# Performance work log

Hardware: AMD Instinct MI355X
Metric: run time of the kernel (lower is better)

The kernel has to match this reference:

```python
import jax, jax.numpy as jnp
import numpy as np

D = 128
N = 300000
M = 262144
LN_EPS = 1e-5


def setup_inputs() -> dict:
    key = jax.random.key(0)
    ks = jax.random.split(key, 20)
    inp = {
        'h_p': jax.random.normal(ks[0], (N, D), jnp.float32),
        'h_k': jax.random.normal(ks[1], (N, D), jnp.float32),
        'h_o': jax.random.normal(ks[2], (M, D), jnp.float32),
        'weight_o': jax.random.normal(ks[3], (D, D // 2), jnp.float32) * 0.15,
        'weight_p': jax.random.normal(ks[4], (D, D // 2), jnp.float32) * 0.15,
        'lin_W': jax.random.normal(ks[5], (D, D), jnp.float32) * 0.08,
        'lin_b': jax.random.normal(ks[6], (D,), jnp.float32) * 0.05,
        'bias': jax.random.normal(ks[7], (D,), jnp.float32) * 0.05,
        'Wq': jax.random.normal(ks[8], (D, D), jnp.float32) * 0.08,
        'bq': jax.random.normal(ks[9], (D,), jnp.float32) * 0.05,
        'Wk': jax.random.normal(ks[10], (D, D), jnp.float32) * 0.08,
        'bk': jax.random.normal(ks[11], (D,), jnp.float32) * 0.05,
        'Wv': jax.random.normal(ks[12], (D, D), jnp.float32) * 0.08,
        'bv': jax.random.normal(ks[13], (D,), jnp.float32) * 0.05,
        'W1': jax.random.normal(ks[14], (D, D), jnp.float32) * 0.08,
        'b1': jax.random.normal(ks[15], (D,), jnp.float32) * 0.05,
        'ln_g': jnp.ones((D,), jnp.float32),
        'ln_b': jnp.zeros((D,), jnp.float32),
        'mutual_index_p': jax.random.randint(ks[16], (M,), 0, N, jnp.int32),
        'mutual_index_k': jax.random.randint(ks[17], (M,), 0, N, jnp.int32),
        'propagation_node_num': N,
        'knowledge_node_num': N,
    }
    return inp


def reference(h_p, h_k, h_o, weight_o, weight_p, lin_W, lin_b, bias,
              Wq, bq, Wk, bk, Wv, bv, W1, b1, ln_g, ln_b,
              mutual_index_p, mutual_index_k,
              propagation_node_num, knowledge_node_num):
    # gather: Q from h_o rows, K from paired h_p/h_k rows (seq len 2)
    ho_sel = h_o[mutual_index_p]                       # [M, D]
    q = ho_sel[:, None, :]                             # [M, 1, D]
    k_in = jnp.stack([h_p[mutual_index_p], h_k[mutual_index_k]], axis=1)  # [M, 2, D]

    Q = q @ Wq.T + bq                                  # [M, 1, D]
    K = k_in @ Wk.T + bk                               # [M, 2, D]
    V = k_in @ Wv.T + bv                               # [M, 2, D]

    scale = jnp.float32(D) ** -0.5
    attn = jax.nn.softmax(jnp.einsum('mqd,mkd->mqk', Q, K) * scale, axis=-1)  # [M,1,2]
    ctx = jnp.einsum('mqk,mkd->mqd', attn, V)          # [M, 1, D]

    fusion = ctx @ W1.T + b1                           # dropout is identity in eval
    mu = jnp.mean(fusion, axis=-1, keepdims=True)
    var = jnp.var(fusion, axis=-1, keepdims=True)
    fusion = (fusion - mu) * jax.lax.rsqrt(var + LN_EPS) * ln_g + ln_b
    fusion = fusion[:, 0, :]                           # [M, D]

    trans_ho = ho_sel @ weight_o                       # [M, D/2]
    trans_pk = fusion @ weight_p                       # [M, D/2]
    out = jnp.tanh(jnp.concatenate([trans_ho, trans_pk], axis=1))
    out = jax.nn.leaky_relu(out @ lin_W.T + lin_b, negative_slope=0.01)
    out = out + bias                                   # [M, D]

    h_p = h_p.at[mutual_index_p].set(out)
    h_k = h_k.at[mutual_index_k].set(out)
    return (h_p, h_k)
```

## Files before the change

### kernel.cpp

```cpp
#include <hip/hip_runtime.h>
#include <stdint.h>

#define D 128
#define NROWS 300000
#define MIDX 262144
#define SBH 132
#define WAVE_BUF (16 * SBH)

typedef __attribute__((ext_vector_type(8))) short short8_t;
typedef __attribute__((ext_vector_type(4))) short short4_t;
typedef __attribute__((ext_vector_type(4))) float float4v;

__device__ __forceinline__ short f2bf(float x) {
  uint32_t u = __float_as_uint(x);
  u = (u + 0x7FFFu + ((u >> 16) & 1u)) >> 16;
  return (short)u;
}

__global__ void winners_kernel(const int* __restrict__ idx_p,
                               const int* __restrict__ idx_k,
                               int* __restrict__ wp, int* __restrict__ wk) {
  int m = blockIdx.x * 256 + threadIdx.x;
  if (m < MIDX) {
    atomicMax(&wp[idx_p[m]], m);
    atomicMax(&wk[idx_k[m]], m);
  }
}

__global__ __launch_bounds__(256)
void copyrest_kernel(const float* __restrict__ h_p, const float* __restrict__ h_k,
                     const int* __restrict__ wp, const int* __restrict__ wk,
                     float* __restrict__ out_p, float* __restrict__ out_k) {
  int g = blockIdx.x * 256 + threadIdx.x;
  int row = g >> 5;
  if (row >= NROWS) return;
  int c = (g & 31) << 2;
  size_t off = (size_t)row * D + c;
  if (wp[row] < 0) *(float4v*)(out_p + off) = *(const float4v*)(h_p + off);
  if (wk[row] < 0) *(float4v*)(out_k + off) = *(const float4v*)(h_k + off);
}

__global__ void pack_kernel(const float* __restrict__ Wq, const float* __restrict__ Wk,
                            const float* __restrict__ Wv, const float* __restrict__ W1,
                            const float* __restrict__ Wl, const float* __restrict__ Wo,
                            const float* __restrict__ Wp, short* __restrict__ dst) {
  int slot = blockIdx.x;
  int lane = threadIdx.x;
  const float* W; int base; int trans; int rel;
  if      (slot < 32)  { W = Wq; base = 0;     trans = 1; rel = slot; }
  else if (slot < 64)  { W = Wk; base = 16384; trans = 1; rel = slot - 32; }
  else if (slot < 96)  { W = Wv; base = 32768; trans = 1; rel = slot - 64; }
  else if (slot < 128) { W = W1; base = 49152; trans = 1; rel = slot - 96; }
  else if (slot < 160) { W = Wl; base = 65536; trans = 1; rel = slot - 128; }
  else if (slot < 176) { W = Wo; base = 81920; trans = 0; rel = slot - 160; }
  else                 { W = Wp; base = 90112; trans = 0; rel = slot - 176; }
  int t = rel >> 2, s = rel & 3;
  int n = 16 * t + (lane & 15);
  int kb = 32 * s + 8 * (lane >> 4);
  short* o = dst + base + (size_t)(rel * 64 + lane) * 8;
  #pragma unroll
  for (int j = 0; j < 8; j++) {
    float v = trans ? W[n * 128 + kb + j] : W[(kb + j) * 64 + n];
    o[j] = f2bf(v);
  }
}

__device__ __forceinline__ float4v gemm_tile(const short8_t a[4], const short* __restrict__ B,
                                             int t, int lane) {
  float4v acc = {0.f, 0.f, 0.f, 0.f};
  #pragma unroll
  for (int s = 0; s < 4; s++) {
    short8_t b = *(const short8_t*)(B + (size_t)((t * 4 + s) * 64 + lane) * 8);
    acc = __builtin_amdgcn_mfma_f32_16x16x32_bf16(a[s], b, acc, 0, 0, 0);
  }
  return acc;
}

__device__ __forceinline__ void load_row_frags(const float* __restrict__ row, int q, short8_t out[4]) {
  #pragma unroll
  for (int s = 0; s < 4; s++) {
    float4v v0 = *(const float4v*)(row + 32 * s + 8 * q);
    float4v v1 = *(const float4v*)(row + 32 * s + 8 * q + 4);
    short8_t r;
    r[0] = f2bf(v0[0]); r[1] = f2bf(v0[1]); r[2] = f2bf(v0[2]); r[3] = f2bf(v0[3]);
    r[4] = f2bf(v1[0]); r[5] = f2bf(v1[1]); r[6] = f2bf(v1[2]); r[7] = f2bf(v1[3]);
    out[s] = r;
  }
}

__device__ __forceinline__ void read_a_frags(const short* __restrict__ sb, int l15, int q, short8_t out[4]) {
  #pragma unroll
  for (int s = 0; s < 4; s++) {
    const short* p = sb + l15 * SBH + 32 * s + 8 * q;
    short4_t lo = *(const short4_t*)p;
    short4_t hi = *(const short4_t*)(p + 4);
    short8_t v;
    v[0] = lo[0]; v[1] = lo[1]; v[2] = lo[2]; v[3] = lo[3];
    v[4] = hi[0]; v[5] = hi[1]; v[6] = hi[2]; v[7] = hi[3];
    out[s] = v;
  }
}

__device__ __forceinline__ float red16(float v) {
  v += __shfl_xor(v, 1);
  v += __shfl_xor(v, 2);
  v += __shfl_xor(v, 4);
  v += __shfl_xor(v, 8);
  return v;
}

__global__ __launch_bounds__(256, 2)
void fused_kernel(const float* __restrict__ h_p, const float* __restrict__ h_k,
                  const float* __restrict__ h_o, int ho_rows,
                  const int* __restrict__ idx_p, const int* __restrict__ idx_k,
                  const short* __restrict__ wbuf,
                  const float* __restrict__ bq, const float* __restrict__ bk,
                  const float* __restrict__ bv, const float* __restrict__ b1,
                  const float* __restrict__ linb, const float* __restrict__ bias,
                  const float* __restrict__ lng, const float* __restrict__ lnb,
                  const int* __restrict__ wp, const int* __restrict__ wk,
                  float* __restrict__ out_p, float* __restrict__ out_k)
{
  const short* Bq_ = wbuf;
  const short* Bk_ = wbuf + 16384;
  const short* Bv_ = wbuf + 32768;
  const short* B1_ = wbuf + 49152;
  const short* Bl_ = wbuf + 65536;
  const short* Bo_ = wbuf + 81920;
  const short* Bp_ = wbuf + 90112;

  __shared__ float smem[4 * WAVE_BUF];
  const int tid  = threadIdx.x;
  const int wave = tid >> 6;
  const int lane = tid & 63;
  const int l15  = lane & 15;
  const int q    = lane >> 4;

  float* fbuf = smem + wave * WAVE_BUF;
  short* sbuf = (short*)fbuf;

  const int m0   = blockIdx.x * 64 + wave * 16;
  const int mrow = m0 + l15;
  const int ip = idx_p[mrow];
  const int ik = idx_k[mrow];
  const int ipo = (ip < ho_rows) ? ip : (ho_rows - 1);

  short8_t aho[4], ahp[4], ahk[4];
  load_row_frags(h_o + (size_t)ipo * D, q, aho);
  load_row_frags(h_p + (size_t)ip * D, q, ahp);
  load_row_frags(h_k + (size_t)ik * D, q, ahk);

  float4v Q[8];
  #pragma unroll
  for (int t = 0; t < 8; t++) {
    Q[t] = gemm_tile(aho, Bq_, t, lane) + bq[16 * t + l15];
  }

  float4v p0 = {0,0,0,0}, p1 = {0,0,0,0};
  #pragma unroll
  for (int t = 0; t < 8; t++) {
    float bkv = bk[16 * t + l15];
    float4v k0 = gemm_tile(ahp, Bk_, t, lane) + bkv;
    float4v k1 = gemm_tile(ahk, Bk_, t, lane) + bkv;
    p0 += Q[t] * k0;
    p1 += Q[t] * k1;
  }
  float a0[4], a1[4];
  #pragma unroll
  for (int r = 0; r < 4; r++) {
    float s0 = red16(p0[r]) * 0.08838834764831845f;
    float s1 = red16(p1[r]) * 0.08838834764831845f;
    float mx = fmaxf(s0, s1);
    float e0 = __expf(s0 - mx), e1 = __expf(s1 - mx);
    float inv = 1.0f / (e0 + e1);
    a0[r] = e0 * inv;
    a1[r] = e1 * inv;
  }

  float4v ctx[8];
  #pragma unroll
  for (int t = 0; t < 8; t++) {
    float bvv = bv[16 * t + l15];
    float4v v0 = gemm_tile(ahp, Bv_, t, lane) + bvv;
    float4v v1 = gemm_tile(ahk, Bv_, t, lane) + bvv;
    float4v c;
    #pragma unroll
    for (int r = 0; r < 4; r++) c[r] = a0[r] * v0[r] + a1[r] * v1[r];
    ctx[t] = c;
  }

  #pragma unroll
  for (int t = 0; t < 8; t++)
    #pragma unroll
    for (int r = 0; r < 4; r++)
      sbuf[(4 * q + r) * SBH + 16 * t + l15] = f2bf(ctx[t][r]);
  short8_t afu[4];
  read_a_frags(sbuf, l15, q, afu);

  float4v F[8];
  float4v sum = {0,0,0,0}, ssq = {0,0,0,0};
  #pragma unroll
  for (int t = 0; t < 8; t++) {
    float4v f = gemm_tile(afu, B1_, t, lane) + b1[16 * t + l15];
    F[t] = f;
    sum += f;
    ssq += f * f;
  }
  #pragma unroll
  for (int r = 0; r < 4; r++) {
    float s  = red16(sum[r]);
    float s2 = red16(ssq[r]);
    float mu  = s * (1.0f / 128.0f);
    float var = s2 * (1.0f / 128.0f) - mu * mu;
    float rs  = rsqrtf(var + 1e-5f);
    #pragma unroll
    for (int t = 0; t < 8; t++) F[t][r] = (F[t][r] - mu) * rs;
  }
  #pragma unroll
  for (int t = 0; t < 8; t++) {
    int col = 16 * t + l15;
    float g = lng[col], b = lnb[col];
    #pragma unroll
    for (int r = 0; r < 4; r++)
      sbuf[(4 * q + r) * SBH + col] = f2bf(F[t][r] * g + b);
  }
  short8_t afn[4];
  read_a_frags(sbuf, l15, q, afn);

  float4v U[8];
  #pragma unroll
  for (int t = 0; t < 4; t++) U[t]     = gemm_tile(aho, Bo_, t, lane);
  #pragma unroll
  for (int t = 0; t < 4; t++) U[4 + t] = gemm_tile(afn, Bp_, t, lane);
  #pragma unroll
  for (int t = 0; t < 8; t++) {
    #pragma unroll
    for (int r = 0; r < 4; r++) {
      float x  = U[t][r];
      float e  = __expf(-2.0f * fabsf(x));
      float th = (1.0f - e) / (1.0f + e);
      sbuf[(4 * q + r) * SBH + 16 * t + l15] = f2bf(copysignf(th, x));
    }
  }
  short8_t au[4];
  read_a_frags(sbuf, l15, q, au);

  #pragma unroll
  for (int t = 0; t < 8; t++) {
    int col = 16 * t + l15;
    float4v z = gemm_tile(au, Bl_, t, lane) + linb[col];
    float bb = bias[col];
    #pragma unroll
    for (int r = 0; r < 4; r++) {
      float x = z[r];
      x = (x > 0.0f) ? x : 0.01f * x;
      fbuf[(4 * q + r) * SBH + col] = x + bb;
    }
  }

  int r_out = lane >> 2;
  int cb    = (lane & 3) * 32;
  int mg    = m0 + r_out;
  int ip2 = idx_p[mg];
  int ik2 = idx_k[mg];
  bool dop = (wp[ip2] == mg);
  bool dok = (wk[ik2] == mg);
  const float* src = fbuf + r_out * SBH + cb;
  float* dp = out_p + (size_t)ip2 * D + cb;
  float* dk = out_k + (size_t)ik2 * D + cb;
  #pragma unroll
  for (int c = 0; c < 32; c += 4) {
    float4v v = *(const float4v*)(src + c);
    if (dop) *(float4v*)(dp + c) = v;
    if (dok) *(float4v*)(dk + c) = v;
  }
}

extern "C" void kernel_launch(void* const* d_in, const int* in_sizes, int n_in,
                              void* d_out, int out_size, void* d_ws, size_t ws_size,
                              hipStream_t stream) {
  const float* h_p      = (const float*)d_in[0];
  const float* h_k      = (const float*)d_in[1];
  const float* h_o      = (const float*)d_in[2];
  const float* weight_o = (const float*)d_in[3];
  const float* weight_p = (const float*)d_in[4];
  const float* lin_W    = (const float*)d_in[5];
  const float* lin_b    = (const float*)d_in[6];
  const float* bias     = (const float*)d_in[7];
  const float* Wq       = (const float*)d_in[8];
  const float* bq       = (const float*)d_in[9];
  const float* Wk       = (const float*)d_in[10];
  const float* bk       = (const float*)d_in[11];
  const float* Wv       = (const float*)d_in[12];
  const float* bv       = (const float*)d_in[13];
  const float* W1       = (const float*)d_in[14];
  const float* b1       = (const float*)d_in[15];
  const float* ln_g     = (const float*)d_in[16];
  const float* ln_b     = (const float*)d_in[17];
  const int*   idx_p    = (const int*)d_in[18];
  const int*   idx_k    = (const int*)d_in[19];

  const int ho_rows = in_sizes[2] / D;

  float* out_p = (float*)d_out;
  float* out_k = out_p + (size_t)NROWS * D;

  int* wp = (int*)d_ws;
  int* wk = wp + NROWS;
  short* wbuf = (short*)((char*)d_ws + (size_t)2 * NROWS * 4);

  hipMemsetAsync(wp, 0xFF, (size_t)2 * NROWS * sizeof(int), stream);

  winners_kernel<<<dim3(MIDX / 256), dim3(256), 0, stream>>>(idx_p, idx_k, wp, wk);
  copyrest_kernel<<<dim3((NROWS * 32 + 255) / 256), dim3(256), 0, stream>>>(
      h_p, h_k, wp, wk, out_p, out_k);
  pack_kernel<<<dim3(192), dim3(64), 0, stream>>>(Wq, Wk, Wv, W1, lin_W, weight_o, weight_p, wbuf);
  fused_kernel<<<dim3(MIDX / 64), dim3(256), 0, stream>>>(
      h_p, h_k, h_o, ho_rows, idx_p, idx_k, wbuf, bq, bk, bv, b1, lin_b, bias, ln_g, ln_b,
      wp, wk, out_p, out_k);
}
```

Baseline: 799.5 us.

## Stage pre-swizzled weight fragments through shared memory with register double-buffering

Each weight matrix fragment set used to be read straight from global memory by every wave. Now the block loads each 32KB weight stage cooperatively into registers, stores it to a shared buffer, and prefetches the next stage while the current GEMM reads from LDS. The aim is to cut redundant global and L2 traffic for the weights. In exchange the kernel adds 32KB of LDS per block, which may lower occupancy, plus many block-wide barriers between stages.

```diff
diff --git a/kernel.cpp b/kernel.cpp
--- a/kernel.cpp
+++ b/kernel.cpp
@@ -65,12 +65,12 @@
   }
 }
 
-__device__ __forceinline__ float4v gemm_tile(const short8_t a[4], const short* __restrict__ B,
-                                             int t, int lane) {
+__device__ __forceinline__ float4v gemm_tile_lds(const short8_t a[4], const short* B,
+                                                 int t, int lane) {
   float4v acc = {0.f, 0.f, 0.f, 0.f};
   #pragma unroll
   for (int s = 0; s < 4; s++) {
-    short8_t b = *(const short8_t*)(B + (size_t)((t * 4 + s) * 64 + lane) * 8);
+    short8_t b = *(const short8_t*)(B + ((t * 4 + s) * 64 + lane) * 8);
     acc = __builtin_amdgcn_mfma_f32_16x16x32_bf16(a[s], b, acc, 0, 0, 0);
   }
   return acc;
@@ -88,7 +88,7 @@
   }
 }
 
-__device__ __forceinline__ void read_a_frags(const short* __restrict__ sb, int l15, int q, short8_t out[4]) {
+__device__ __forceinline__ void read_a_frags(const short* sb, int l15, int q, short8_t out[4]) {
   #pragma unroll
   for (int s = 0; s < 4; s++) {
     const short* p = sb + l15 * SBH + 32 * s + 8 * q;
@@ -127,9 +127,10 @@
   const short* B1_ = wbuf + 49152;
   const short* Bl_ = wbuf + 65536;
   const short* Bo_ = wbuf + 81920;
-  const short* Bp_ = wbuf + 90112;
-
+
+  __shared__ short bsh[16384];
   __shared__ float smem[4 * WAVE_BUF];
+
   const int tid  = threadIdx.x;
   const int wave = tid >> 6;
   const int lane = tid & 63;
@@ -150,18 +151,35 @@
   load_row_frags(h_p + (size_t)ip * D, q, ahp);
   load_row_frags(h_k + (size_t)ik * D, q, ahk);
 
+  short8_t breg[8];
+
+  #define LDSTAGE(SRC) { _Pragma("unroll") \
+    for (int r_ = 0; r_ < 8; r_++) breg[r_] = *(const short8_t*)((SRC) + (r_ * 256 + tid) * 8); }
+  #define STSTAGE() { _Pragma("unroll") \
+    for (int r_ = 0; r_ < 8; r_++) *(short8_t*)(bsh + (r_ * 256 + tid) * 8) = breg[r_]; }
+
+  LDSTAGE(Bq_);
+  STSTAGE();
+  LDSTAGE(Bk_);
+  __syncthreads();
+
   float4v Q[8];
   #pragma unroll
   for (int t = 0; t < 8; t++) {
-    Q[t] = gemm_tile(aho, Bq_, t, lane) + bq[16 * t + l15];
-  }
+    Q[t] = gemm_tile_lds(aho, bsh, t, lane) + bq[16 * t + l15];
+  }
+
+  __syncthreads();
+  STSTAGE();
+  LDSTAGE(Bv_);
+  __syncthreads();
 
   float4v p0 = {0,0,0,0}, p1 = {0,0,0,0};
   #pragma unroll
   for (int t = 0; t < 8; t++) {
     float bkv = bk[16 * t + l15];
-    float4v k0 = gemm_tile(ahp, Bk_, t, lane) + bkv;
-    float4v k1 = gemm_tile(ahk, Bk_, t, lane) + bkv;
+    float4v k0 = gemm_tile_lds(ahp, bsh, t, lane) + bkv;
+    float4v k1 = gemm_tile_lds(ahk, bsh, t, lane) + bkv;
     p0 += Q[t] * k0;
     p1 += Q[t] * k1;
   }
@@ -177,12 +195,17 @@
     a1[r] = e1 * inv;
   }
 
+  __syncthreads();
+  STSTAGE();
+  LDSTAGE(B1_);
+  __syncthreads();
+
   float4v ctx[8];
   #pragma unroll
   for (int t = 0; t < 8; t++) {
     float bvv = bv[16 * t + l15];
-    float4v v0 = gemm_tile(ahp, Bv_, t, lane) + bvv;
-    float4v v1 = gemm_tile(ahk, Bv_, t, lane) + bvv;
+    float4v v0 = gemm_tile_lds(ahp, bsh, t, lane) + bvv;
+    float4v v1 = gemm_tile_lds(ahk, bsh, t, lane) + bvv;
     float4v c;
     #pragma unroll
     for (int r = 0; r < 4; r++) c[r] = a0[r] * v0[r] + a1[r] * v1[r];
@@ -197,11 +220,16 @@
   short8_t afu[4];
   read_a_frags(sbuf, l15, q, afu);
 
+  __syncthreads();
+  STSTAGE();
+  LDSTAGE(Bo_);
+  __syncthreads();
+
   float4v F[8];
   float4v sum = {0,0,0,0}, ssq = {0,0,0,0};
   #pragma unroll
   for (int t = 0; t < 8; t++) {
-    float4v f = gemm_tile(afu, B1_, t, lane) + b1[16 * t + l15];
+    float4v f = gemm_tile_lds(afu, bsh, t, lane) + b1[16 * t + l15];
     F[t] = f;
     sum += f;
     ssq += f * f;
@@ -227,11 +255,16 @@
   short8_t afn[4];
   read_a_frags(sbuf, l15, q, afn);
 
+  __syncthreads();
+  STSTAGE();
+  LDSTAGE(Bl_);
+  __syncthreads();
+
   float4v U[8];
   #pragma unroll
-  for (int t = 0; t < 4; t++) U[t]     = gemm_tile(aho, Bo_, t, lane);
-  #pragma unroll
-  for (int t = 0; t < 4; t++) U[4 + t] = gemm_tile(afn, Bp_, t, lane);
+  for (int t = 0; t < 4; t++) U[t]     = gemm_tile_lds(aho, bsh, t, lane);
+  #pragma unroll
+  for (int t = 0; t < 4; t++) U[4 + t] = gemm_tile_lds(afn, bsh + 8192, t, lane);
   #pragma unroll
   for (int t = 0; t < 8; t++) {
     #pragma unroll
@@ -245,10 +278,14 @@
   short8_t au[4];
   read_a_frags(sbuf, l15, q, au);
 
+  __syncthreads();
+  STSTAGE();
+  __syncthreads();
+
   #pragma unroll
   for (int t = 0; t < 8; t++) {
     int col = 16 * t + l15;
-    float4v z = gemm_tile(au, Bl_, t, lane) + linb[col];
+    float4v z = gemm_tile_lds(au, bsh, t, lane) + linb[col];
     float bb = bias[col];
     #pragma unroll
     for (int r = 0; r < 4; r++) {
@@ -274,6 +311,8 @@
     if (dop) *(float4v*)(dp + c) = v;
     if (dok) *(float4v*)(dk + c) = v;
   }
+  #undef LDSTAGE
+  #undef STSTAGE
 }
 
 extern "C" void kernel_launch(void* const* d_in, const int* in_sizes, int n_in,
```

After: 763.0 us. -4.6%, faster.
